# Kernel tuning notes

Hardware: AMD Instinct MI355X
Metric: run time of the kernel (lower is better)

## Reference

```python
import jax, jax.numpy as jnp
import numpy as np

D_MODEL = 2048
N_HEADS = 16
N_KV_HEADS = 4
HEAD_DIM = D_MODEL // N_HEADS  # 128
ROPE_BASE = 10000.0


def _rope_tables(T, head_dim):
    half = head_dim // 2
    theta = 1.0 / (ROPE_BASE ** (jnp.arange(half, dtype=jnp.float32) / half))
    m = jnp.arange(T, dtype=jnp.float32)
    freqs = jnp.outer(m, theta)  # (T, half)
    return jnp.cos(freqs), jnp.sin(freqs)


def _apply_rope(x, cos, sin):
    # x: (B, H, T, hd); rotate first/second halves as pairs
    half = x.shape[-1] // 2
    x1, x2 = x[..., :half], x[..., half:]
    cos = cos[None, None, :, :]
    sin = sin[None, None, :, :]
    return jnp.concatenate([x1 * cos - x2 * sin, x1 * sin + x2 * cos], axis=-1)


def setup_inputs() -> dict:
    key = jax.random.key(0)
    ks = jax.random.split(key, 5)
    B, T = 4, 2048
    x = jax.random.normal(ks[0], (B, T, D_MODEL), dtype=jnp.float32)
    Wq = jax.random.normal(ks[1], (D_MODEL, N_HEADS * HEAD_DIM), dtype=jnp.float32) * 0.02
    Wk = jax.random.normal(ks[2], (D_MODEL, N_KV_HEADS * HEAD_DIM), dtype=jnp.float32) * 0.02
    Wv = jax.random.normal(ks[3], (D_MODEL, N_KV_HEADS * HEAD_DIM), dtype=jnp.float32) * 0.02
    Wo = jax.random.normal(ks[4], (N_HEADS * HEAD_DIM, D_MODEL), dtype=jnp.float32) * (0.02 / np.sqrt(2.0))
    return {"x": x, "Wq": Wq, "Wk": Wk, "Wv": Wv, "Wo": Wo}


def reference(x, Wq, Wk, Wv, Wo):
    B, T, C = x.shape
    groups = N_HEADS // N_KV_HEADS

    # QKV projections
    q = (x @ Wq).reshape(B, T, N_HEADS, HEAD_DIM).transpose(0, 2, 1, 3)      # (B,H,T,hd)
    k = (x @ Wk).reshape(B, T, N_KV_HEADS, HEAD_DIM).transpose(0, 2, 1, 3)   # (B,Hkv,T,hd)
    v = (x @ Wv).reshape(B, T, N_KV_HEADS, HEAD_DIM).transpose(0, 2, 1, 3)

    # RoPE on q and k
    cos, sin = _rope_tables(T, HEAD_DIM)
    q = _apply_rope(q, cos, sin)
    k = _apply_rope(k, cos, sin)

    # GQA: repeat each kv head `groups` times
    k = jnp.repeat(k, groups, axis=1)  # (B,H,T,hd)
    v = jnp.repeat(v, groups, axis=1)

    # Attention scores with ALiBi bias and causal mask
    scale = 1.0 / np.sqrt(HEAD_DIM)
    scores = jnp.einsum('bhqd,bhkd->bhqk', q, k) * scale  # (B,H,T,T)

    pos = jnp.arange(T)
    dist = jnp.minimum(pos[None, :] - pos[:, None], 0).astype(jnp.float32)  # (T,T), <=0
    slopes = 2.0 ** (-8.0 * jnp.arange(1, N_HEADS + 1, dtype=jnp.float32) / N_HEADS)
    alibi = slopes[:, None, None] * dist[None, :, :]  # (H,T,T)
    scores = scores + alibi[None]

    causal = pos[None, :] > pos[:, None]  # True = future = blocked
    scores = jnp.where(causal[None, None], -jnp.inf, scores)

    weights = jax.nn.softmax(scores, axis=-1)
    out = jnp.einsum('bhqk,bhkd->bhqd', weights, v)  # (B,H,T,hd)
    out = out.transpose(0, 2, 1, 3).reshape(B, T, N_HEADS * HEAD_DIM)
    return out @ Wo
```

## Files before the change

kernel.cpp:

```cpp
#include <hip/hip_runtime.h>
#include <hip/hip_bf16.h>
#include <stdint.h>

#define T_SEQ 2048
#define DM    2048
#define NH    16
#define NKVH  4
#define HD    128
#define NBATCH 4
#define BT    (NBATCH * T_SEQ)
#define ATT_SCALE 0.08838834764831845f
#define LOG2E 1.4426950408889634f

typedef __attribute__((ext_vector_type(8))) short bf16x8;
typedef __attribute__((ext_vector_type(4))) float f32x4;
typedef __attribute__((ext_vector_type(16))) float f32x16;
typedef __attribute__((ext_vector_type(8))) unsigned short ushort8;
typedef __attribute__((ext_vector_type(4))) unsigned short ushort4v;

static __device__ __forceinline__ unsigned short f2bf(float f) {
  __hip_bfloat16 h = __float2bfloat16(f);
  return __builtin_bit_cast(unsigned short, h);
}
static __device__ __forceinline__ float bf2f(unsigned short u) {
  unsigned int v = ((unsigned int)u) << 16;
  return __builtin_bit_cast(float, v);
}
static __device__ __forceinline__ unsigned int packbf2(float a, float b) {
  return (unsigned int)f2bf(a) | ((unsigned int)f2bf(b) << 16);
}

#define GLDS16(g, l)                                                        \
  __builtin_amdgcn_global_load_lds(                                         \
      (const __attribute__((address_space(1))) void*)(g),                   \
      (__attribute__((address_space(3))) void*)(l), 16, 0, 0)

__global__ __launch_bounds__(256) void castx_k(const float* __restrict__ x,
                                               unsigned short* __restrict__ xb) {
  int i = (blockIdx.x * 256 + threadIdx.x) * 4;
  float4 v = *(const float4*)&x[i];
  ushort4v o;
  o[0] = f2bf(v.x); o[1] = f2bf(v.y); o[2] = f2bf(v.z); o[3] = f2bf(v.w);
  *(ushort4v*)&xb[i] = o;
}

__global__ __launch_bounds__(256) void transw_k(const float* __restrict__ src,
                                                unsigned short* __restrict__ dst,
                                                int ncols) {
  __shared__ unsigned short t[64][72];
  int n0 = blockIdx.x * 64, r0 = blockIdx.y * 64;
  int tid = threadIdx.x;
  int tx = tid & 15, ty = tid >> 4;
#pragma unroll
  for (int i = 0; i < 4; i++) {
    int r = ty * 4 + i;
    float4 v = *(const float4*)&src[(size_t)(r0 + r) * ncols + n0 + tx * 4];
    t[r][tx * 4 + 0] = f2bf(v.x);
    t[r][tx * 4 + 1] = f2bf(v.y);
    t[r][tx * 4 + 2] = f2bf(v.z);
    t[r][tx * 4 + 3] = f2bf(v.w);
  }
  __syncthreads();
  int nl = tid >> 2, seg = tid & 3;
  ushort8 o0, o1;
#pragma unroll
  for (int j = 0; j < 8; j++) {
    o0[j] = t[seg * 16 + j][nl];
    o1[j] = t[seg * 16 + 8 + j][nl];
  }
  size_t base = (size_t)(n0 + nl) * 2048 + r0 + seg * 16;
  *(ushort8*)&dst[base] = o0;
  *(ushort8*)&dst[base + 8] = o1;
}

template <int EPI>
__global__ __launch_bounds__(256) void gemm_k(const unsigned short* __restrict__ A,
                                              const unsigned short* __restrict__ Bt,
                                              unsigned short* __restrict__ q_out,
                                              unsigned short* __restrict__ k_out,
                                              unsigned short* __restrict__ v_out,
                                              float* __restrict__ f_out) {
  __shared__ unsigned short As[128 * 32];
  __shared__ unsigned short Bs[128 * 32];
  const int tid = threadIdx.x;
  const int lane = tid & 63;
  const int wid = tid >> 6;
  const int wr = wid >> 1, wc = wid & 1;
  const int row0 = blockIdx.x * 128, n00 = blockIdx.y * 128;
  const int lr = lane & 15, lk = (lane >> 4) * 8;
  const int c0 = tid, c1 = tid + 256;

  f32x4 acc[4][4] = {};

  for (int k0 = 0; k0 < 2048; k0 += 32) {
    __syncthreads();
    GLDS16(A + (size_t)(row0 + (c0 >> 2)) * 2048 + k0 + (c0 & 3) * 8, &As[c0 * 8]);
    GLDS16(A + (size_t)(row0 + (c1 >> 2)) * 2048 + k0 + (c1 & 3) * 8, &As[c1 * 8]);
    GLDS16(Bt + (size_t)(n00 + (c0 >> 2)) * 2048 + k0 + (c0 & 3) * 8, &Bs[c0 * 8]);
    GLDS16(Bt + (size_t)(n00 + (c1 >> 2)) * 2048 + k0 + (c1 & 3) * 8, &Bs[c1 * 8]);
    __syncthreads();
    bf16x8 af[4], bfr[4];
#pragma unroll
    for (int mi = 0; mi < 4; mi++)
      af[mi] = *(const bf16x8*)&As[(wr * 64 + mi * 16 + lr) * 32 + lk];
#pragma unroll
    for (int ni = 0; ni < 4; ni++)
      bfr[ni] = *(const bf16x8*)&Bs[(wc * 64 + ni * 16 + lr) * 32 + lk];
#pragma unroll
    for (int mi = 0; mi < 4; mi++)
#pragma unroll
      for (int ni = 0; ni < 4; ni++)
        acc[mi][ni] =
            __builtin_amdgcn_mfma_f32_16x16x32_bf16(af[mi], bfr[ni], acc[mi][ni], 0, 0, 0);
  }

  const int rbase = row0 + wr * 64;
  const int cbase = n00 + wc * 64;
#pragma unroll
  for (int mi = 0; mi < 4; mi++)
#pragma unroll
    for (int ni = 0; ni < 4; ni++)
#pragma unroll
      for (int r = 0; r < 4; r++) {
        int row = rbase + mi * 16 + (lane >> 4) * 4 + r;
        int col = cbase + ni * 16 + lr;
        float v = acc[mi][ni][r];
        if (EPI == 0) {
          if (col < 2048) {
            q_out[(size_t)row * 2048 + col] = f2bf(v);
          } else if (col < 2560) {
            k_out[(size_t)row * 512 + (col - 2048)] = f2bf(v);
          } else {
            int nv = col - 2560;
            int kvh = nv >> 7, d = nv & 127;
            int b = row >> 11, tt = row & 2047;
            v_out[((size_t)(b * NKVH + kvh) * HD + d) * T_SEQ + tt] = f2bf(v);
          }
        } else {
          f_out[(size_t)row * 2048 + col] = v;
        }
      }
}

__global__ __launch_bounds__(256) void rope_k(unsigned short* __restrict__ qb,
                                              unsigned short* __restrict__ kb) {
  int idx = blockIdx.x * 256 + threadIdx.x;
  int i = idx & 63;
  int wi = idx >> 6;
  int hh = wi % (NH + NKVH);
  int bt = wi / (NH + NKVH);
  int t = bt & (T_SEQ - 1);
  unsigned short* p = (hh < NH) ? (qb + (size_t)bt * 2048 + hh * HD)
                                : (kb + (size_t)bt * 512 + (hh - NH) * HD);
  float theta = exp2f(-(float)i * (13.287712379549449f / 64.0f));
  float ang = (float)t * theta;
  float s, c;
  sincosf(ang, &s, &c);
  float x1 = bf2f(p[i]), x2 = bf2f(p[i + 64]);
  p[i] = f2bf(x1 * c - x2 * s);
  p[i + 64] = f2bf(x1 * s + x2 * c);
}

__global__ __launch_bounds__(256) void attn_k(const unsigned short* __restrict__ qb,
                                              const unsigned short* __restrict__ kb,
                                              const unsigned short* __restrict__ vt,
                                              unsigned short* __restrict__ ao) {
  __shared__ __align__(16) unsigned short smem[17408];

  const int bid = blockIdx.x;
  const int p = bid & 7;
  const int h = (bid >> 3) & 15;
  const int b = bid >> 7;
  const int tid = threadIdx.x;
  const int wid = tid >> 6, lane = tid & 63;
  const int l31 = lane & 31, lh = lane >> 5;
  const int kvh = h >> 2;
  const float slope2 = exp2f(-0.5f * (float)(h + 1)) * LOG2E;
  const float scale2 = ATT_SCALE * LOG2E;

  const int krow = tid >> 4;
  const int kchunk = tid & 15;
  const int cgk = kchunk ^ (krow & 7);
  const int vrow = tid >> 2;
  const int vchunk = tid & 3;
  const int cgv = vchunk ^ (vrow & 3);
  const int kxor = l31 & 7;
  const int vxor = l31 & 3;

  const unsigned short* khead = kb + (size_t)(b * T_SEQ) * 512 + kvh * 128;
  const unsigned short* vhead = vt + (size_t)(b * NKVH + kvh) * HD * T_SEQ;

  auto stage = [&](int buf, int k0) {
#pragma unroll
    for (int c = 0; c < 2; c++)
      GLDS16(khead + (size_t)(k0 + c * 16 + krow) * 512 + cgk * 8,
             &smem[buf * 4096 + c * 2048 + tid * 8]);
#pragma unroll
    for (int c = 0; c < 2; c++)
      GLDS16(vhead + (size_t)(c * 64 + vrow) * T_SEQ + k0 + cgv * 8,
             &smem[8192 + buf * 4096 + c * 2048 + tid * 8]);
  };

  unsigned short (*ot)[32][136] = (unsigned short(*)[32][136])smem;

#pragma unroll 1
  for (int half = 0; half < 2; ++half) {
    const int j = half ? (15 - p) : p;
    const int q0 = j * 128 + wid * 32;
    const int dt_w = j * 4 + wid;
    const int T_blk = j * 4 + 4;

    const unsigned short* qrow =
        qb + ((size_t)(b * T_SEQ + q0 + l31)) * 2048 + h * HD + lh * 8;
    bf16x8 qf[8];
#pragma unroll
    for (int ds = 0; ds < 8; ds++) qf[ds] = *(const bf16x8*)&qrow[ds * 16];

    f32x16 oacc[4] = {};
    float m2 = -1e30f, l_sum = 0.f;

    __syncthreads();
    stage(0, 0);
    __syncthreads();
    int cur = 0;

#pragma unroll 1
    for (int t = 0; t < T_blk; ++t) {
      if (t + 1 < T_blk) stage(cur ^ 1, 32 * (t + 1));

      if (t <= dt_w) {
        const int k0 = t * 32;
        const unsigned short* Kb = &smem[cur * 4096];
        const unsigned short* Vb = &smem[8192 + cur * 4096];

        bf16x8 kf[8];
#pragma unroll
        for (int ds = 0; ds < 8; ds++)
          kf[ds] = *(const bf16x8*)&Kb[l31 * 128 + ((2 * ds + lh) ^ kxor) * 8];
        bf16x8 vf[4][2];
#pragma unroll
        for (int dt = 0; dt < 4; dt++)
#pragma unroll
          for (int ks = 0; ks < 2; ks++)
            vf[dt][ks] =
                *(const bf16x8*)&Vb[(dt * 32 + l31) * 32 + ((2 * ks + lh) ^ vxor) * 8];

        __builtin_amdgcn_s_setprio(1);
        f32x16 sca = 0.f, scb = 0.f;
#pragma unroll
        for (int ds = 0; ds < 4; ds++)
          sca = __builtin_amdgcn_mfma_f32_32x32x16_bf16(kf[ds], qf[ds], sca, 0, 0, 0);
#pragma unroll
        for (int ds = 4; ds < 8; ds++)
          scb = __builtin_amdgcn_mfma_f32_32x32x16_bf16(kf[ds], qf[ds], scb, 0, 0, 0);
        __builtin_amdgcn_s_setprio(0);

        float s[16];
        const float ab = slope2 * (float)k0;
        const bool diag = (t == dt_w);
#pragma unroll
        for (int r = 0; r < 16; r++) {
          const int crow = (r & 3) + 8 * (r >> 2) + 4 * lh;
          float v = fmaf(sca[r] + scb[r], scale2, fmaf(slope2, (float)crow, ab));
          if (diag && crow > l31) v = -1e30f;
          s[r] = v;
        }

        float t8[8], t4[4];
#pragma unroll
        for (int i = 0; i < 8; i++) t8[i] = fmaxf(s[i], s[i + 8]);
#pragma unroll
        for (int i = 0; i < 4; i++) t4[i] = fmaxf(t8[i], t8[i + 4]);
        float mx = fmaxf(fmaxf(t4[0], t4[1]), fmaxf(t4[2], t4[3]));
        mx = fmaxf(mx, __shfl_xor(mx, 32));
        const float m2new = fmaxf(m2, mx);
        const float corr = exp2f(m2 - m2new);

        float pr[16];
#pragma unroll
        for (int r = 0; r < 16; r++) pr[r] = exp2f(s[r] - m2new);

        float a8[8], a4[4];
#pragma unroll
        for (int i = 0; i < 8; i++) a8[i] = pr[i] + pr[i + 8];
#pragma unroll
        for (int i = 0; i < 4; i++) a4[i] = a8[i] + a8[i + 4];
        float rs = (a4[0] + a4[1]) + (a4[2] + a4[3]);
        rs += __shfl_xor(rs, 32);
        l_sum = l_sum * corr + rs;
        m2 = m2new;

#pragma unroll
        for (int dt = 0; dt < 4; dt++) oacc[dt] *= corr;

        unsigned int w[8];
#pragma unroll
        for (int i = 0; i < 8; i++) w[i] = packbf2(pr[2 * i], pr[2 * i + 1]);
        const unsigned int ta = __shfl_xor(lh ? w[0] : w[2], 32);
        const unsigned int tb = __shfl_xor(lh ? w[1] : w[3], 32);
        const unsigned int tc = __shfl_xor(lh ? w[4] : w[6], 32);
        const unsigned int td = __shfl_xor(lh ? w[5] : w[7], 32);
        union U4 { unsigned int u[4]; bf16x8 v; } f0, f1;
        f0.u[0] = lh ? ta : w[0];
        f0.u[1] = lh ? tb : w[1];
        f0.u[2] = lh ? w[2] : ta;
        f0.u[3] = lh ? w[3] : tb;
        f1.u[0] = lh ? tc : w[4];
        f1.u[1] = lh ? td : w[5];
        f1.u[2] = lh ? w[6] : tc;
        f1.u[3] = lh ? w[7] : td;

        __builtin_amdgcn_s_setprio(1);
#pragma unroll
        for (int dt = 0; dt < 4; dt++) {
          oacc[dt] =
              __builtin_amdgcn_mfma_f32_32x32x16_bf16(vf[dt][0], f0.v, oacc[dt], 0, 0, 0);
          oacc[dt] =
              __builtin_amdgcn_mfma_f32_32x32x16_bf16(vf[dt][1], f1.v, oacc[dt], 0, 0, 0);
        }
        __builtin_amdgcn_s_setprio(0);
      }

      __syncthreads();
      cur ^= 1;
    }

    const float inv = 1.0f / l_sum;
#pragma unroll
    for (int dt = 0; dt < 4; dt++)
#pragma unroll
      for (int rg = 0; rg < 4; rg++) {
        ushort4v o;
#pragma unroll
        for (int jj = 0; jj < 4; jj++) o[jj] = f2bf(oacc[dt][rg * 4 + jj] * inv);
        *(ushort4v*)&ot[wid][l31][dt * 32 + rg * 8 + lh * 4] = o;
      }
    __syncthreads();
    const int rrow = lane >> 4, chunk = lane & 15;
#pragma unroll
    for (int ps = 0; ps < 8; ps++) {
      const int row = ps * 4 + rrow;
      ushort8 v = *(const ushort8*)&ot[wid][row][chunk * 8];
      *(ushort8*)&ao[((size_t)(b * T_SEQ + q0 + row)) * 2048 + h * HD + chunk * 8] = v;
    }
  }
}

extern "C" void kernel_launch(void* const* d_in, const int* in_sizes, int n_in,
                              void* d_out, int out_size, void* d_ws, size_t ws_size,
                              hipStream_t stream) {
  const float* x = (const float*)d_in[0];
  const float* Wq = (const float*)d_in[1];
  const float* Wk = (const float*)d_in[2];
  const float* Wv = (const float*)d_in[3];
  const float* Wo = (const float*)d_in[4];

  char* w = (char*)d_ws;
  unsigned short* xb = (unsigned short*)w;
  unsigned short* wqt = (unsigned short*)(w + 33554432);
  unsigned short* qb = (unsigned short*)(w + 33554432 + 12582912);
  unsigned short* kb = (unsigned short*)(w + 33554432 + 12582912 + 33554432);
  unsigned short* vtb = (unsigned short*)(w + 33554432 + 12582912 + 33554432 + 8388608);

  castx_k<<<16384, 256, 0, stream>>>(x, xb);
  transw_k<<<dim3(32, 32), 256, 0, stream>>>(Wq, wqt, 2048);
  transw_k<<<dim3(8, 32), 256, 0, stream>>>(Wk, wqt + (size_t)2048 * 2048, 512);
  transw_k<<<dim3(8, 32), 256, 0, stream>>>(Wv, wqt + (size_t)2560 * 2048, 512);
  gemm_k<0><<<dim3(64, 24), 256, 0, stream>>>(xb, wqt, qb, kb, vtb, nullptr);
  rope_k<<<40960, 256, 0, stream>>>(qb, kb);
  transw_k<<<dim3(32, 32), 256, 0, stream>>>(Wo, wqt, 2048);
  attn_k<<<512, 256, 0, stream>>>(qb, kb, vtb, xb);
  gemm_k<1><<<dim3(64, 16), 256, 0, stream>>>(xb, wqt, nullptr, nullptr, nullptr,
                                              (float*)d_out);
}
```

Measured before the change: 525.9 us.

## Reschedule attention blocks longest-first, reverse KV order, and skip most rescalings

The attention kernel no longer pairs two query tiles per block. It launches one block per query tile, ordered from the longest causal range to the shortest, and groups heads that share a KV head so they tend to run together and reuse K/V in cache. KV tiles are now processed from the diagonal backward, so the large ALiBi-biased scores come first, and the online-softmax rescale only runs when the max grows by more than a threshold (lazy rescaling). V fragment loads also move after the QK MFMAs. The trade-off is twice as many blocks, and the lazy threshold lets exponentials exceed 1, which is safe in fp32 but changes rounding slightly.

```diff
diff --git a/kernel.cpp b/kernel.cpp
--- a/kernel.cpp
+++ b/kernel.cpp
@@ -168,15 +168,25 @@
   __shared__ __align__(16) unsigned short smem[17408];
 
   const int bid = blockIdx.x;
-  const int p = bid & 7;
-  const int h = (bid >> 3) & 15;
-  const int b = bid >> 7;
+  const int level = bid >> 6;
+  const int j = 15 - level;
+  const int rr = bid & 63;
+  const int s8 = rr & 7;
+  const int w8 = rr >> 3;
+  const int g = s8 + 8 * (w8 & 1);
+  const int hh = w8 >> 1;
+  const int b = g >> 2, kvh = g & 3;
+  const int h = kvh * 4 + hh;
+
   const int tid = threadIdx.x;
   const int wid = tid >> 6, lane = tid & 63;
   const int l31 = lane & 31, lh = lane >> 5;
-  const int kvh = h >> 2;
   const float slope2 = exp2f(-0.5f * (float)(h + 1)) * LOG2E;
   const float scale2 = ATT_SCALE * LOG2E;
+
+  const int q0 = j * 128 + wid * 32;
+  const int dt_w = j * 4 + wid;
+  const int T_blk = j * 4 + 4;
 
   const int krow = tid >> 4;
   const int kchunk = tid & 15;
@@ -203,146 +213,143 @@
 
   unsigned short (*ot)[32][136] = (unsigned short(*)[32][136])smem;
 
+  const unsigned short* qrow =
+      qb + ((size_t)(b * T_SEQ + q0 + l31)) * 2048 + h * HD + lh * 8;
+  bf16x8 qf[8];
+#pragma unroll
+  for (int ds = 0; ds < 8; ds++) qf[ds] = *(const bf16x8*)&qrow[ds * 16];
+
+  f32x16 oacc[4] = {};
+  float m2 = -1e30f, l_sum = 0.f;
+  const float arow = -slope2 * (float)(q0 + l31);
+
+  stage(0, 32 * (T_blk - 1));
+  __syncthreads();
+  int cur = 0;
+
 #pragma unroll 1
-  for (int half = 0; half < 2; ++half) {
-    const int j = half ? (15 - p) : p;
-    const int q0 = j * 128 + wid * 32;
-    const int dt_w = j * 4 + wid;
-    const int T_blk = j * 4 + 4;
-
-    const unsigned short* qrow =
-        qb + ((size_t)(b * T_SEQ + q0 + l31)) * 2048 + h * HD + lh * 8;
-    bf16x8 qf[8];
-#pragma unroll
-    for (int ds = 0; ds < 8; ds++) qf[ds] = *(const bf16x8*)&qrow[ds * 16];
-
-    f32x16 oacc[4] = {};
-    float m2 = -1e30f, l_sum = 0.f;
+  for (int it = 0; it < T_blk; ++it) {
+    const int tt = T_blk - 1 - it;
+    if (it + 1 < T_blk) stage(cur ^ 1, 32 * (tt - 1));
+
+    if (tt <= dt_w) {
+      const int k0 = tt * 32;
+      const unsigned short* Kb = &smem[cur * 4096];
+      const unsigned short* Vb = &smem[8192 + cur * 4096];
+
+      bf16x8 kf[8];
+#pragma unroll
+      for (int ds = 0; ds < 8; ds++)
+        kf[ds] = *(const bf16x8*)&Kb[l31 * 128 + ((2 * ds + lh) ^ kxor) * 8];
+
+      __builtin_amdgcn_s_setprio(1);
+      f32x16 sca = 0.f, scb = 0.f;
+#pragma unroll
+      for (int ds = 0; ds < 4; ds++)
+        sca = __builtin_amdgcn_mfma_f32_32x32x16_bf16(kf[ds], qf[ds], sca, 0, 0, 0);
+#pragma unroll
+      for (int ds = 4; ds < 8; ds++)
+        scb = __builtin_amdgcn_mfma_f32_32x32x16_bf16(kf[ds], qf[ds], scb, 0, 0, 0);
+      __builtin_amdgcn_s_setprio(0);
+
+      bf16x8 vf[4][2];
+#pragma unroll
+      for (int dt = 0; dt < 4; dt++)
+#pragma unroll
+        for (int ks = 0; ks < 2; ks++)
+          vf[dt][ks] =
+              *(const bf16x8*)&Vb[(dt * 32 + l31) * 32 + ((2 * ks + lh) ^ vxor) * 8];
+
+      float s[16];
+      const float ab = fmaf(slope2, (float)k0, arow);
+      const bool diag = (tt == dt_w);
+#pragma unroll
+      for (int r = 0; r < 16; r++) {
+        const int crow = (r & 3) + 8 * (r >> 2) + 4 * lh;
+        float v = fmaf(sca[r] + scb[r], scale2, fmaf(slope2, (float)crow, ab));
+        if (diag && crow > l31) v = -1e30f;
+        s[r] = v;
+      }
+
+      float t8[8], t4[4];
+#pragma unroll
+      for (int i = 0; i < 8; i++) t8[i] = fmaxf(s[i], s[i + 8]);
+#pragma unroll
+      for (int i = 0; i < 4; i++) t4[i] = fmaxf(t8[i], t8[i + 4]);
+      float mx = fmaxf(fmaxf(t4[0], t4[1]), fmaxf(t4[2], t4[3]));
+      mx = fmaxf(mx, __shfl_xor(mx, 32));
+
+      if (__any(mx > m2 + 8.f)) {
+        const float mnew = fmaxf(m2, mx);
+        const float corr = exp2f(m2 - mnew);
+        l_sum *= corr;
+#pragma unroll
+        for (int dt = 0; dt < 4; dt++) oacc[dt] *= corr;
+        m2 = mnew;
+      }
+
+      float pr[16];
+#pragma unroll
+      for (int r = 0; r < 16; r++) pr[r] = exp2f(s[r] - m2);
+
+      float a8[8], a4[4];
+#pragma unroll
+      for (int i = 0; i < 8; i++) a8[i] = pr[i] + pr[i + 8];
+#pragma unroll
+      for (int i = 0; i < 4; i++) a4[i] = a8[i] + a8[i + 4];
+      float rs = (a4[0] + a4[1]) + (a4[2] + a4[3]);
+      rs += __shfl_xor(rs, 32);
+      l_sum += rs;
+
+      unsigned int w[8];
+#pragma unroll
+      for (int i = 0; i < 8; i++) w[i] = packbf2(pr[2 * i], pr[2 * i + 1]);
+      const unsigned int ta = __shfl_xor(lh ? w[0] : w[2], 32);
+      const unsigned int tb = __shfl_xor(lh ? w[1] : w[3], 32);
+      const unsigned int tc = __shfl_xor(lh ? w[4] : w[6], 32);
+      const unsigned int td = __shfl_xor(lh ? w[5] : w[7], 32);
+      union U4 { unsigned int u[4]; bf16x8 v; } f0, f1;
+      f0.u[0] = lh ? ta : w[0];
+      f0.u[1] = lh ? tb : w[1];
+      f0.u[2] = lh ? w[2] : ta;
+      f0.u[3] = lh ? w[3] : tb;
+      f1.u[0] = lh ? tc : w[4];
+      f1.u[1] = lh ? td : w[5];
+      f1.u[2] = lh ? w[6] : tc;
+      f1.u[3] = lh ? w[7] : td;
+
+      __builtin_amdgcn_s_setprio(1);
+#pragma unroll
+      for (int dt = 0; dt < 4; dt++) {
+        oacc[dt] =
+            __builtin_amdgcn_mfma_f32_32x32x16_bf16(vf[dt][0], f0.v, oacc[dt], 0, 0, 0);
+        oacc[dt] =
+            __builtin_amdgcn_mfma_f32_32x32x16_bf16(vf[dt][1], f1.v, oacc[dt], 0, 0, 0);
+      }
+      __builtin_amdgcn_s_setprio(0);
+    }
 
     __syncthreads();
-    stage(0, 0);
-    __syncthreads();
-    int cur = 0;
-
-#pragma unroll 1
-    for (int t = 0; t < T_blk; ++t) {
-      if (t + 1 < T_blk) stage(cur ^ 1, 32 * (t + 1));
-
-      if (t <= dt_w) {
-        const int k0 = t * 32;
-        const unsigned short* Kb = &smem[cur * 4096];
-        const unsigned short* Vb = &smem[8192 + cur * 4096];
-
-        bf16x8 kf[8];
-#pragma unroll
-        for (int ds = 0; ds < 8; ds++)
-          kf[ds] = *(const bf16x8*)&Kb[l31 * 128 + ((2 * ds + lh) ^ kxor) * 8];
-        bf16x8 vf[4][2];
-#pragma unroll
-        for (int dt = 0; dt < 4; dt++)
-#pragma unroll
-          for (int ks = 0; ks < 2; ks++)
-            vf[dt][ks] =
-                *(const bf16x8*)&Vb[(dt * 32 + l31) * 32 + ((2 * ks + lh) ^ vxor) * 8];
-
-        __builtin_amdgcn_s_setprio(1);
-        f32x16 sca = 0.f, scb = 0.f;
-#pragma unroll
-        for (int ds = 0; ds < 4; ds++)
-          sca = __builtin_amdgcn_mfma_f32_32x32x16_bf16(kf[ds], qf[ds], sca, 0, 0, 0);
-#pragma unroll
-        for (int ds = 4; ds < 8; ds++)
-          scb = __builtin_amdgcn_mfma_f32_32x32x16_bf16(kf[ds], qf[ds], scb, 0, 0, 0);
-        __builtin_amdgcn_s_setprio(0);
-
-        float s[16];
-        const float ab = slope2 * (float)k0;
-        const bool diag = (t == dt_w);
-#pragma unroll
-        for (int r = 0; r < 16; r++) {
-          const int crow = (r & 3) + 8 * (r >> 2) + 4 * lh;
-          float v = fmaf(sca[r] + scb[r], scale2, fmaf(slope2, (float)crow, ab));
-          if (diag && crow > l31) v = -1e30f;
-          s[r] = v;
-        }
-
-        float t8[8], t4[4];
-#pragma unroll
-        for (int i = 0; i < 8; i++) t8[i] = fmaxf(s[i], s[i + 8]);
-#pragma unroll
-        for (int i = 0; i < 4; i++) t4[i] = fmaxf(t8[i], t8[i + 4]);
-        float mx = fmaxf(fmaxf(t4[0], t4[1]), fmaxf(t4[2], t4[3]));
-        mx = fmaxf(mx, __shfl_xor(mx, 32));
-        const float m2new = fmaxf(m2, mx);
-        const float corr = exp2f(m2 - m2new);
-
-        float pr[16];
-#pragma unroll
-        for (int r = 0; r < 16; r++) pr[r] = exp2f(s[r] - m2new);
-
-        float a8[8], a4[4];
-#pragma unroll
-        for (int i = 0; i < 8; i++) a8[i] = pr[i] + pr[i + 8];
-#pragma unroll
-        for (int i = 0; i < 4; i++) a4[i] = a8[i] + a8[i + 4];
-        float rs = (a4[0] + a4[1]) + (a4[2] + a4[3]);
-        rs += __shfl_xor(rs, 32);
-        l_sum = l_sum * corr + rs;
-        m2 = m2new;
-
-#pragma unroll
-        for (int dt = 0; dt < 4; dt++) oacc[dt] *= corr;
-
-        unsigned int w[8];
-#pragma unroll
-        for (int i = 0; i < 8; i++) w[i] = packbf2(pr[2 * i], pr[2 * i + 1]);
-        const unsigned int ta = __shfl_xor(lh ? w[0] : w[2], 32);
-        const unsigned int tb = __shfl_xor(lh ? w[1] : w[3], 32);
-        const unsigned int tc = __shfl_xor(lh ? w[4] : w[6], 32);
-        const unsigned int td = __shfl_xor(lh ? w[5] : w[7], 32);
-        union U4 { unsigned int u[4]; bf16x8 v; } f0, f1;
-        f0.u[0] = lh ? ta : w[0];
-        f0.u[1] = lh ? tb : w[1];
-        f0.u[2] = lh ? w[2] : ta;
-        f0.u[3] = lh ? w[3] : tb;
-        f1.u[0] = lh ? tc : w[4];
-        f1.u[1] = lh ? td : w[5];
-        f1.u[2] = lh ? w[6] : tc;
-        f1.u[3] = lh ? w[7] : td;
-
-        __builtin_amdgcn_s_setprio(1);
-#pragma unroll
-        for (int dt = 0; dt < 4; dt++) {
-          oacc[dt] =
-              __builtin_amdgcn_mfma_f32_32x32x16_bf16(vf[dt][0], f0.v, oacc[dt], 0, 0, 0);
-          oacc[dt] =
-              __builtin_amdgcn_mfma_f32_32x32x16_bf16(vf[dt][1], f1.v, oacc[dt], 0, 0, 0);
-        }
-        __builtin_amdgcn_s_setprio(0);
-      }
-
-      __syncthreads();
-      cur ^= 1;
+    cur ^= 1;
+  }
+
+  const float inv = 1.0f / l_sum;
+#pragma unroll
+  for (int dt = 0; dt < 4; dt++)
+#pragma unroll
+    for (int rg = 0; rg < 4; rg++) {
+      ushort4v o;
+#pragma unroll
+      for (int jj = 0; jj < 4; jj++) o[jj] = f2bf(oacc[dt][rg * 4 + jj] * inv);
+      *(ushort4v*)&ot[wid][l31][dt * 32 + rg * 8 + lh * 4] = o;
     }
-
-    const float inv = 1.0f / l_sum;
-#pragma unroll
-    for (int dt = 0; dt < 4; dt++)
-#pragma unroll
-      for (int rg = 0; rg < 4; rg++) {
-        ushort4v o;
-#pragma unroll
-        for (int jj = 0; jj < 4; jj++) o[jj] = f2bf(oacc[dt][rg * 4 + jj] * inv);
-        *(ushort4v*)&ot[wid][l31][dt * 32 + rg * 8 + lh * 4] = o;
-      }
-    __syncthreads();
-    const int rrow = lane >> 4, chunk = lane & 15;
-#pragma unroll
-    for (int ps = 0; ps < 8; ps++) {
-      const int row = ps * 4 + rrow;
-      ushort8 v = *(const ushort8*)&ot[wid][row][chunk * 8];
-      *(ushort8*)&ao[((size_t)(b * T_SEQ + q0 + row)) * 2048 + h * HD + chunk * 8] = v;
-    }
+  __syncthreads();
+  const int rrow = lane >> 4, chunk = lane & 15;
+#pragma unroll
+  for (int ps = 0; ps < 8; ps++) {
+    const int row = ps * 4 + rrow;
+    ushort8 v = *(const ushort8*)&ot[wid][row][chunk * 8];
+    *(ushort8*)&ao[((size_t)(b * T_SEQ + q0 + row)) * 2048 + h * HD + chunk * 8] = v;
   }
 }
 
@@ -369,7 +376,7 @@
   gemm_k<0><<<dim3(64, 24), 256, 0, stream>>>(xb, wqt, qb, kb, vtb, nullptr);
   rope_k<<<40960, 256, 0, stream>>>(qb, kb);
   transw_k<<<dim3(32, 32), 256, 0, stream>>>(Wo, wqt, 2048);
-  attn_k<<<512, 256, 0, stream>>>(qb, kb, vtb, xb);
+  attn_k<<<1024, 256, 0, stream>>>(qb, kb, vtb, xb);
   gemm_k<1><<<dim3(64, 16), 256, 0, stream>>>(xb, wqt, nullptr, nullptr, nullptr,
                                               (float*)d_out);
 }
```

After: 486.7 us. 1.08x faster.
